# Kernel tuning notes

Measured on AMD Instinct MI355X. Metric: run time of the kernel, lower is better.

## Reference

```python
import jax, jax.numpy as jnp
import numpy as np

B, N, C, H, AD, HID = 2, 1024, 768, 12, 8, 3072
SCALE = (C // H) ** -0.5


def setup_inputs() -> dict:
    key = jax.random.key(0)
    ks = jax.random.split(key, 32)
    inp = {}
    for i in range(5):
        inp[f"x{i}"] = jax.random.normal(ks[i], (B, N, C), jnp.float32)
    def w(i, shape, s=0.02):
        return jax.random.normal(ks[i], shape, jnp.float32) * s
    inp.update({
        "ln1_g": jnp.ones((C,), jnp.float32), "ln1_b": jnp.zeros((C,), jnp.float32),
        "ln2_g": jnp.ones((C,), jnp.float32), "ln2_b": jnp.zeros((C,), jnp.float32),
        "qkv_w": w(5, (C, 3 * C)), "qkv_b": jnp.zeros((3 * C,), jnp.float32),
        "proj_w": w(6, (C, C)), "proj_b": jnp.zeros((C,), jnp.float32),
        "fc1_w": w(7, (C, HID)), "fc1_b": jnp.zeros((HID,), jnp.float32),
        "fc2_w": w(8, (HID, C)), "fc2_b": jnp.zeros((C,), jnp.float32),
        "at_dw": w(9, (C, AD)), "at_db": jnp.zeros((AD,), jnp.float32),
        "at_mw": w(10, (AD, AD)), "at_mb": jnp.zeros((AD,), jnp.float32),
        "at_uw": w(11, (AD, C)), "at_ub": jnp.zeros((C,), jnp.float32),
        "a2_dw": w(12, (C, AD)), "a2_db": jnp.zeros((AD,), jnp.float32),
        "a2_mw": w(13, (AD, AD)), "a2_mb": jnp.zeros((AD,), jnp.float32),
        "a2_uw": w(14, (AD, C)), "a2_ub": jnp.zeros((C,), jnp.float32),
    })
    return inp


def _ln(x, g, b, eps=1e-5):
    mu = x.mean(-1, keepdims=True)
    xc = x - mu
    var = (xc * xc).mean(-1, keepdims=True)
    return xc * jax.lax.rsqrt(var + eps) * g + b


def _adapter(x, dw, db, mw, mb, uw, ub):
    h = x @ dw + db          # bottleneck down [., AD]
    h = h @ mw + mb          # mid
    return h @ uw + ub       # up back to C


def _attn(x, qkv_w, qkv_b, proj_w, proj_b):
    # x: [S, B, N, C] (streams folded in leading axis)
    s, b, n, c = x.shape
    qkv = (x @ qkv_w + qkv_b).reshape(s, b, n, 3, H, c // H)
    q, k, v = jnp.moveaxis(qkv, 3, 0)            # each [S,B,N,H,D]
    scores = jnp.einsum('sbnhd,sbmhd->sbhnm', q * SCALE, k)  # fp32; clamp is a no-op
    p = jax.nn.softmax(scores, axis=-1)
    o = jnp.einsum('sbhnm,sbmhd->sbnhd', p, v).reshape(s, b, n, c)
    return o @ proj_w + proj_b


def reference(x0, x1, x2, x3, x4,
              ln1_g, ln1_b, ln2_g, ln2_b,
              qkv_w, qkv_b, proj_w, proj_b,
              fc1_w, fc1_b, fc2_w, fc2_b,
              at_dw, at_db, at_mw, at_mb, at_uw, at_ub,
              a2_dw, a2_db, a2_mw, a2_mb, a2_uw, a2_ub):
    xs = jnp.stack([x0, x1, x2, x3, x4])          # [5,B,N,C]
    n1 = _ln(xs, ln1_g, ln1_b)
    a1 = _adapter(n1, at_dw, at_db, at_mw, at_mb, at_uw, at_ub)
    ao = _attn(n1, qkv_w, qkv_b, proj_w, proj_b)
    # cross-stream residuals: x01=a1[0], x12=a1[1], ..., x10=a1[1], x21=a1[2], ...
    y0 = xs[0] + ao[0] + a1[1]
    y1 = xs[1] + ao[1] + a1[0] + a1[2]
    y2 = xs[2] + ao[2] + a1[1] + a1[3]
    y3 = xs[3] + ao[3] + a1[2] + a1[4]
    y4 = xs[4] + ao[4] + a1[3]
    ys = jnp.stack([y0, y1, y2, y3, y4])
    a2 = _adapter(_ln(ys, ln1_g, ln1_b), a2_dw, a2_db, a2_mw, a2_mb, a2_uw, a2_ub)
    h = _ln(ys, ln2_g, ln2_b) @ fc1_w + fc1_b
    m = jax.nn.gelu(h, approximate=False) @ fc2_w + fc2_b
    z0 = ys[0] + m[0] + a2[1]
    z1 = ys[1] + m[1] + a2[0] + a2[2]
    z2 = ys[2] + m[2] + a2[1] + a2[3]
    z3 = ys[3] + m[3] + a2[2] + a2[4]
    z4 = ys[4] + m[4] + a2[3]
    return jnp.stack([z0, z1, z2, z3, z4])        # [5,B,N,C]
```

## Files before the change

kernel.cpp:

```cpp
#include <hip/hip_runtime.h>
#include <math.h>

typedef __bf16 bf16;
typedef __attribute__((ext_vector_type(8))) __bf16 bf16x8;
typedef __attribute__((ext_vector_type(4))) __bf16 bf16x4;
typedef __attribute__((ext_vector_type(4))) float f32x4;
typedef __attribute__((ext_vector_type(16))) float f32x16;

#define TOK   10240
#define CD    768
#define NQKV  2304
#define NHID  3072
#define SEQ   1024
#define NH    12

__device__ __forceinline__ f32x4 mfma16(bf16x8 a, bf16x8 b, f32x4 c) {
  return __builtin_amdgcn_mfma_f32_16x16x32_bf16(a, b, c, 0, 0, 0);
}
__device__ __forceinline__ f32x16 mfma32(bf16x8 a, bf16x8 b, f32x16 c) {
  return __builtin_amdgcn_mfma_f32_32x32x16_bf16(a, b, c, 0, 0, 0);
}

__device__ __forceinline__ void gload16(const void* g, void* l) {
  __builtin_amdgcn_global_load_lds(
      (const __attribute__((address_space(1))) void*)g,
      (__attribute__((address_space(3))) void*)l, 16, 0, 0);
}

__device__ __forceinline__ unsigned pack2(bf16 a, bf16 b) {
  union { unsigned short u[2]; unsigned v; } x;
  x.u[0] = __builtin_bit_cast(unsigned short, a);
  x.u[1] = __builtin_bit_cast(unsigned short, b);
  return x.v;
}

__device__ __forceinline__ float fast_gelu(float v) {
  float u = 0.7978845608f * (v + 0.044715f * v * v * v);
  float e = __expf(fminf(2.f * u, 30.f));
  return 0.5f * v * (1.f + (e - 1.f) / (e + 1.f));
}

__global__ __launch_bounds__(256) void transpose_to_bf16(
    const float* __restrict__ in, bf16* __restrict__ out, int K, int N) {
  __shared__ float tile[32][33];
  const int bn = blockIdx.x * 32, bk = blockIdx.y * 32;
  const int r = threadIdx.x >> 5, c = threadIdx.x & 31;
#pragma unroll
  for (int i = 0; i < 4; ++i)
    tile[r + 8 * i][c] = in[(size_t)(bk + r + 8 * i) * N + bn + c];
  __syncthreads();
#pragma unroll
  for (int i = 0; i < 4; ++i)
    out[(size_t)(bn + r + 8 * i) * K + bk + c] = (bf16)tile[c][r + 8 * i];
}

__global__ __launch_bounds__(256) void ln5_kernel(
    const float* __restrict__ x0, const float* __restrict__ x1,
    const float* __restrict__ x2, const float* __restrict__ x3,
    const float* __restrict__ x4, const float* __restrict__ g,
    const float* __restrict__ b, bf16* __restrict__ out) {
  const int w = threadIdx.x >> 6, lane = threadIdx.x & 63;
  const int row = blockIdx.x * 4 + w;
  const int s = row >> 11, rem = row & 2047;
  const float* xp;
  switch (s) {
    case 0: xp = x0; break; case 1: xp = x1; break; case 2: xp = x2; break;
    case 3: xp = x3; break; default: xp = x4; break;
  }
  const f32x4* xr = (const f32x4*)(xp + (size_t)rem * CD);
  f32x4 v[3];
#pragma unroll
  for (int i = 0; i < 3; ++i) v[i] = xr[lane + 64 * i];
  float sum = 0.f;
#pragma unroll
  for (int i = 0; i < 3; ++i)
#pragma unroll
    for (int j = 0; j < 4; ++j) sum += v[i][j];
#pragma unroll
  for (int m = 32; m >= 1; m >>= 1) sum += __shfl_xor(sum, m);
  const float mu = sum * (1.f / 768.f);
  float vs = 0.f;
#pragma unroll
  for (int i = 0; i < 3; ++i)
#pragma unroll
    for (int j = 0; j < 4; ++j) { float d = v[i][j] - mu; vs += d * d; }
#pragma unroll
  for (int m = 32; m >= 1; m >>= 1) vs += __shfl_xor(vs, m);
  const float rstd = rsqrtf(vs * (1.f / 768.f) + 1e-5f);
  const f32x4* gp = (const f32x4*)g;
  const f32x4* bp = (const f32x4*)b;
  bf16* orow = out + (size_t)row * CD;
#pragma unroll
  for (int i = 0; i < 3; ++i) {
    const int c4 = lane + 64 * i;
    f32x4 gg = gp[c4], bb = bp[c4];
    bf16x4 o;
#pragma unroll
    for (int j = 0; j < 4; ++j)
      o[j] = (bf16)((v[i][j] - mu) * rstd * gg[j] + bb[j]);
    *(bf16x4*)(orow + c4 * 4) = o;
  }
}

__global__ __launch_bounds__(256) void fuse_res_ln(
    const float* __restrict__ x0, const float* __restrict__ x1,
    const float* __restrict__ x2, const float* __restrict__ x3,
    const float* __restrict__ x4, const float* __restrict__ add,
    const float* __restrict__ a, float* __restrict__ ys,
    const float* __restrict__ g1, const float* __restrict__ b1,
    const float* __restrict__ g2, const float* __restrict__ b2,
    bf16* __restrict__ o1, bf16* __restrict__ o2) {
  const int w = threadIdx.x >> 6, lane = threadIdx.x & 63;
  const int row = blockIdx.x * 4 + w;
  const int s = row >> 11, rem = row & 2047;
  const float* xp;
  switch (s) {
    case 0: xp = x0; break; case 1: xp = x1; break; case 2: xp = x2; break;
    case 3: xp = x3; break; default: xp = x4; break;
  }
  const f32x4* xr = (const f32x4*)(xp + (size_t)rem * CD);
  const f32x4* ar = (const f32x4*)(add + (size_t)row * CD);
  const f32x4* am = (const f32x4*)(a + (size_t)(row - 2048) * CD);
  const f32x4* ap = (const f32x4*)(a + (size_t)(row + 2048) * CD);
  f32x4 v[3];
#pragma unroll
  for (int i = 0; i < 3; ++i) {
    const int c4 = lane + 64 * i;
    f32x4 t = xr[c4] + ar[c4];
    if (s > 0) t += am[c4];
    if (s < 4) t += ap[c4];
    v[i] = t;
  }
  f32x4* yr = (f32x4*)(ys + (size_t)row * CD);
#pragma unroll
  for (int i = 0; i < 3; ++i) yr[lane + 64 * i] = v[i];

  float sum = 0.f;
#pragma unroll
  for (int i = 0; i < 3; ++i)
#pragma unroll
    for (int j = 0; j < 4; ++j) sum += v[i][j];
#pragma unroll
  for (int m = 32; m >= 1; m >>= 1) sum += __shfl_xor(sum, m);
  const float mu = sum * (1.f / 768.f);
  float vs = 0.f;
#pragma unroll
  for (int i = 0; i < 3; ++i)
#pragma unroll
    for (int j = 0; j < 4; ++j) { float d = v[i][j] - mu; vs += d * d; }
#pragma unroll
  for (int m = 32; m >= 1; m >>= 1) vs += __shfl_xor(vs, m);
  const float rstd = rsqrtf(vs * (1.f / 768.f) + 1e-5f);
  bf16* r1 = o1 + (size_t)row * CD;
  bf16* r2 = o2 + (size_t)row * CD;
#pragma unroll
  for (int i = 0; i < 3; ++i) {
    const int c4 = lane + 64 * i;
    f32x4 gg1 = ((const f32x4*)g1)[c4], bb1 = ((const f32x4*)b1)[c4];
    f32x4 gg2 = ((const f32x4*)g2)[c4], bb2 = ((const f32x4*)b2)[c4];
    bf16x4 oa, ob;
#pragma unroll
    for (int j = 0; j < 4; ++j) {
      float n = (v[i][j] - mu) * rstd;
      oa[j] = (bf16)(n * gg1[j] + bb1[j]);
      ob[j] = (bf16)(n * gg2[j] + bb2[j]);
    }
    *(bf16x4*)(r1 + c4 * 4) = oa;
    *(bf16x4*)(r2 + c4 * 4) = ob;
  }
}

template <int EPI>
__global__ __launch_bounds__(256) void gemm_bt(
    const bf16* __restrict__ A, const bf16* __restrict__ Bt,
    const float* __restrict__ bias, void* __restrict__ Cout, int N, int K,
    int nbn) {
  __shared__ bf16 As[2][4096];
  __shared__ bf16 Bs[2][4096];
  const int t = threadIdx.x, lane = t & 63, w = t >> 6;
  const int wm = w >> 1, wn = w & 1;

  const int chunk = gridDim.x >> 3;
  const int wg = (blockIdx.x & 7) * chunk + (blockIdx.x >> 3);
  const int bm = wg / nbn, bn = wg % nbn;

  f32x4 acc[4][4] = {};

  const int srow = t >> 2;
  const int scol = ((t & 3) ^ (srow & 3)) << 3;
  const bf16* a0 = A + (size_t)(bm * 128 + srow) * K + scol;
  const bf16* b0 = Bt + (size_t)(bn * 128 + srow) * K + scol;
  const size_t rstride = (size_t)64 * K;

  const int arow = wm * 64 + (lane & 15);
  const int brow = wn * 64 + (lane & 15);
  const int pch = (((lane >> 4) ^ (lane & 3)) << 3);

  gload16(a0, &As[0][w * 512]);
  gload16(a0 + rstride, &As[0][2048 + w * 512]);
  gload16(b0, &Bs[0][w * 512]);
  gload16(b0 + rstride, &Bs[0][2048 + w * 512]);
  __syncthreads();

  int cur = 0;
  for (int kt = 0; kt < K; kt += 32) {
    if (kt + 32 < K) {
      const bf16* ak = a0 + kt + 32;
      const bf16* bk = b0 + kt + 32;
      gload16(ak, &As[cur ^ 1][w * 512]);
      gload16(ak + rstride, &As[cur ^ 1][2048 + w * 512]);
      gload16(bk, &Bs[cur ^ 1][w * 512]);
      gload16(bk + rstride, &Bs[cur ^ 1][2048 + w * 512]);
    }
    bf16x8 af[4], bfr[4];
#pragma unroll
    for (int f = 0; f < 4; ++f) {
      af[f] = *(const bf16x8*)&As[cur][(arow + f * 16) * 32 + pch];
      bfr[f] = *(const bf16x8*)&Bs[cur][(brow + f * 16) * 32 + pch];
    }
#pragma unroll
    for (int mf = 0; mf < 4; ++mf)
#pragma unroll
      for (int nf = 0; nf < 4; ++nf)
        acc[mf][nf] = mfma16(af[mf], bfr[nf], acc[mf][nf]);
    __syncthreads();
    cur ^= 1;
  }

#pragma unroll
  for (int mf = 0; mf < 4; ++mf) {
    const int grow0 = bm * 128 + wm * 64 + mf * 16 + (lane >> 4) * 4;
#pragma unroll
    for (int nf = 0; nf < 4; ++nf) {
      const int gcol = bn * 128 + wn * 64 + nf * 16 + (lane & 15);
      const float bv = bias[gcol];
#pragma unroll
      for (int r = 0; r < 4; ++r) {
        float v = acc[mf][nf][r] + bv;
        if (EPI == 2) v = fast_gelu(v);
        const size_t idx = (size_t)(grow0 + r) * N + gcol;
        if (EPI == 0) ((float*)Cout)[idx] = v;
        else ((bf16*)Cout)[idx] = (bf16)v;
      }
    }
  }
}

__global__ __launch_bounds__(256, 3) void attn_v2(
    const bf16* __restrict__ qkv, bf16* __restrict__ obuf) {
  __shared__ bf16 Ks[2][4096];
  __shared__ bf16 Vt[2][4096];
  const int t = threadIdx.x, lane = t & 63, w = t >> 6;
  const int g = lane >> 5, q32 = lane & 31, rq7 = q32 & 7;

  const int xcd = blockIdx.x & 7, slot = blockIdx.x >> 3;
  const int work = xcd * 120 + slot;
  const int sbh = work >> 3, qt = work & 7;
  const int sb = sbh / NH, h = sbh % NH;
  const size_t tokbase = (size_t)sb * SEQ;
  const int qoff = h * 64, koff = CD + h * 64, voff = 2 * CD + h * 64;

  const int qrow = qt * 128 + w * 32 + q32;
  bf16x8 qf[4];
  {
    const bf16* qp = qkv + (tokbase + qrow) * NQKV + qoff + g * 8;
#pragma unroll
    for (int kd = 0; kd < 4; ++kd) {
      bf16x8 v = *(const bf16x8*)(qp + kd * 16);
#pragma unroll
      for (int j = 0; j < 8; ++j) v[j] = (bf16)((float)v[j] * 0.125f);
      qf[kd] = v;
    }
  }

  const int skv1 = t >> 3, sc1 = (t & 7) ^ (skv1 & 7);
  const int skv2 = (t + 256) >> 3, sc2 = (t & 7) ^ (skv2 & 7);
  const int vkv0 = 2 * (t & 31);
  const int vd0 = 8 * (t >> 5);
  const int c0 = (vkv0 & 51) | ((vkv0 & 4) << 1) | ((vkv0 & 8) >> 1);
  const int vchunk = c0 >> 3, vsub = c0 & 7;
  const bf16* kbase = qkv + tokbase * NQKV + koff;
  const bf16* vbase = qkv + tokbase * NQKV + voff;

  {
    const bf16* kb0 = kbase;
    gload16(kb0 + (size_t)skv1 * NQKV + sc1 * 8, &Ks[0][w * 512]);
    gload16(kb0 + (size_t)skv2 * NQKV + sc2 * 8, &Ks[0][2048 + w * 512]);
    const bf16* vp = vbase + (size_t)vkv0 * NQKV + vd0;
    bf16x8 r0 = *(const bf16x8*)vp;
    bf16x8 r1 = *(const bf16x8*)(vp + NQKV);
#pragma unroll
    for (int j = 0; j < 8; ++j) {
      const int d = vd0 + j;
      *(unsigned*)&Vt[0][d * 64 + ((vchunk ^ j) << 3) + vsub] =
          pack2(r0[j], r1[j]);
    }
  }
  __syncthreads();

  float m_run = -1e30f, l_run = 0.f;
  f32x16 oT0 = {}, oT1 = {};
  int cur = 0;

  for (int kt = 0; kt < 16; ++kt) {
    bf16x8 nv0, nv1;
    if (kt < 15) {
      const bf16* vp = vbase + (size_t)((kt + 1) * 64 + vkv0) * NQKV + vd0;
      nv0 = *(const bf16x8*)vp;
      nv1 = *(const bf16x8*)(vp + NQKV);
      const bf16* kb0 = kbase + (size_t)(kt + 1) * 64 * NQKV;
      gload16(kb0 + (size_t)skv1 * NQKV + sc1 * 8, &Ks[cur ^ 1][w * 512]);
      gload16(kb0 + (size_t)skv2 * NQKV + sc2 * 8,
              &Ks[cur ^ 1][2048 + w * 512]);
    }

    f32x16 sT0 = {}, sT1 = {};
#pragma unroll
    for (int kd = 0; kd < 4; ++kd) {
      bf16x8 kf0 =
          *(const bf16x8*)&Ks[cur][q32 * 64 + (((2 * kd + g) ^ rq7) << 3)];
      bf16x8 kf1 = *(const bf16x8*)&Ks[cur][(32 + q32) * 64 +
                                            (((2 * kd + g) ^ rq7) << 3)];
      sT0 = mfma32(kf0, qf[kd], sT0);
      sT1 = mfma32(kf1, qf[kd], sT1);
    }

    float mt = sT0[0];
#pragma unroll
    for (int r = 1; r < 16; ++r) mt = fmaxf(mt, sT0[r]);
#pragma unroll
    for (int r = 0; r < 16; ++r) mt = fmaxf(mt, sT1[r]);
    mt = fmaxf(mt, __shfl_xor(mt, 32));
    const float mnew = fmaxf(m_run, mt);
    const float alpha = __expf(m_run - mnew);
    m_run = mnew;
    float rs = 0.f;
#pragma unroll
    for (int r = 0; r < 16; ++r) {
      sT0[r] = __expf(sT0[r] - mnew);
      rs += sT0[r];
    }
#pragma unroll
    for (int r = 0; r < 16; ++r) {
      sT1[r] = __expf(sT1[r] - mnew);
      rs += sT1[r];
    }
    rs += __shfl_xor(rs, 32);
    l_run = l_run * alpha + rs;
#pragma unroll
    for (int r = 0; r < 16; ++r) { oT0[r] *= alpha; oT1[r] *= alpha; }

    bf16x8 pa[4];
#pragma unroll
    for (int hh = 0; hh < 2; ++hh)
#pragma unroll
      for (int j = 0; j < 8; ++j) {
        pa[hh][j] = (bf16)sT0[8 * hh + j];
        pa[2 + hh][j] = (bf16)sT1[8 * hh + j];
      }

#pragma unroll
    for (int ks = 0; ks < 4; ++ks) {
      bf16x8 vf0 =
          *(const bf16x8*)&Vt[cur][q32 * 64 + (((2 * ks + g) ^ rq7) << 3)];
      bf16x8 vf1 = *(const bf16x8*)&Vt[cur][(32 + q32) * 64 +
                                            (((2 * ks + g) ^ rq7) << 3)];
      oT0 = mfma32(vf0, pa[ks], oT0);
      oT1 = mfma32(vf1, pa[ks], oT1);
    }

    if (kt < 15) {
#pragma unroll
      for (int j = 0; j < 8; ++j) {
        const int d = vd0 + j;
        *(unsigned*)&Vt[cur ^ 1][d * 64 + ((vchunk ^ j) << 3) + vsub] =
            pack2(nv0[j], nv1[j]);
      }
    }
    __syncthreads();
    cur ^= 1;
  }

  const float rl = 1.f / l_run;
  bf16* orow = obuf + (tokbase + qrow) * CD + h * 64;
#pragma unroll
  for (int m = 0; m < 4; ++m) {
    bf16x4 o0, o1;
#pragma unroll
    for (int r = 0; r < 4; ++r) {
      o0[r] = (bf16)(oT0[4 * m + r] * rl);
      o1[r] = (bf16)(oT1[4 * m + r] * rl);
    }
    *(bf16x4*)(orow + 8 * m + 4 * g) = o0;
    *(bf16x4*)(orow + 32 + 8 * m + 4 * g) = o1;
  }
}

__global__ __launch_bounds__(256) void adapter_kernel(
    const bf16* __restrict__ X, const float* __restrict__ dw,
    const float* __restrict__ db, const float* __restrict__ mw,
    const float* __restrict__ mb, const float* __restrict__ uw,
    const float* __restrict__ ub, float* __restrict__ out) {
  const int tok = blockIdx.x * 4 + (threadIdx.x >> 6);
  const int lane = threadIdx.x & 63;
  const bf16* xr = X + (size_t)tok * CD;
  float xv[12];
#pragma unroll
  for (int i = 0; i < 12; ++i) xv[i] = (float)xr[lane + 64 * i];
  float h1[8] = {0, 0, 0, 0, 0, 0, 0, 0};
#pragma unroll
  for (int i = 0; i < 12; ++i) {
    const f32x4* dr = (const f32x4*)(dw + (size_t)(lane + 64 * i) * 8);
    f32x4 d0 = dr[0], d1 = dr[1];
#pragma unroll
    for (int j = 0; j < 4; ++j) {
      h1[j] += xv[i] * d0[j];
      h1[4 + j] += xv[i] * d1[j];
    }
  }
#pragma unroll
  for (int m = 1; m < 64; m <<= 1)
#pragma unroll
    for (int j = 0; j < 8; ++j) h1[j] += __shfl_xor(h1[j], m);
#pragma unroll
  for (int j = 0; j < 8; ++j) h1[j] += db[j];
  float h2[8];
#pragma unroll
  for (int k = 0; k < 8; ++k) {
    float v = mb[k];
#pragma unroll
    for (int j = 0; j < 8; ++j) v += h1[j] * mw[j * 8 + k];
    h2[k] = v;
  }
#pragma unroll
  for (int i = 0; i < 12; ++i) {
    const int c = lane + 64 * i;
    float v = ub[c];
#pragma unroll
    for (int k = 0; k < 8; ++k) v += h2[k] * uw[k * CD + c];
    out[(size_t)tok * CD + c] = v;
  }
}

__global__ __launch_bounds__(256) void cross_residual(
    const float* __restrict__ p0, const float* __restrict__ p1,
    const float* __restrict__ p2, const float* __restrict__ p3,
    const float* __restrict__ p4, const float* __restrict__ add,
    const float* __restrict__ a, float* __restrict__ out) {
  const int s = blockIdx.y;
  const size_t i = (size_t)blockIdx.x * 256 + threadIdx.x;
  const size_t spitch = (size_t)2048 * 768 / 4;
  const size_t sb = (size_t)s * spitch;
  const float* p;
  switch (s) {
    case 0: p = p0; break; case 1: p = p1; break; case 2: p = p2; break;
    case 3: p = p3; break; default: p = p4; break;
  }
  f32x4 v = ((const f32x4*)p)[i];
  v += ((const f32x4*)add)[sb + i];
  if (s > 0) v += ((const f32x4*)a)[sb - spitch + i];
  if (s < 4) v += ((const f32x4*)a)[sb + spitch + i];
  ((f32x4*)out)[sb + i] = v;
}

#define OFF_WTQKV  ((size_t)0)
#define OFF_WTPROJ ((size_t)3538944)
#define OFF_WTFC1  ((size_t)4718592)
#define OFF_WTFC2  ((size_t)9437184)
#define OFF_N1     ((size_t)14155776)
#define OFF_BIG    ((size_t)29884416)
#define OFF_OBUF   ((size_t)77070336)
#define OFF_AOM    ((size_t)92798976)
#define OFF_A12    ((size_t)124256256)
#define OFF_YS     ((size_t)155713536)
#define OFF_L2Y    ((size_t)187170816)

extern "C" void kernel_launch(void* const* d_in, const int* in_sizes, int n_in,
                              void* d_out, int out_size, void* d_ws,
                              size_t ws_size, hipStream_t stream) {
  const float* x0 = (const float*)d_in[0];
  const float* x1 = (const float*)d_in[1];
  const float* x2 = (const float*)d_in[2];
  const float* x3 = (const float*)d_in[3];
  const float* x4 = (const float*)d_in[4];
  const float* ln1_g = (const float*)d_in[5];
  const float* ln1_b = (const float*)d_in[6];
  const float* ln2_g = (const float*)d_in[7];
  const float* ln2_b = (const float*)d_in[8];
  const float* qkv_w = (const float*)d_in[9];
  const float* qkv_b = (const float*)d_in[10];
  const float* proj_w = (const float*)d_in[11];
  const float* proj_b = (const float*)d_in[12];
  const float* fc1_w = (const float*)d_in[13];
  const float* fc1_b = (const float*)d_in[14];
  const float* fc2_w = (const float*)d_in[15];
  const float* fc2_b = (const float*)d_in[16];
  const float* at_dw = (const float*)d_in[17];
  const float* at_db = (const float*)d_in[18];
  const float* at_mw = (const float*)d_in[19];
  const float* at_mb = (const float*)d_in[20];
  const float* at_uw = (const float*)d_in[21];
  const float* at_ub = (const float*)d_in[22];
  const float* a2_dw = (const float*)d_in[23];
  const float* a2_db = (const float*)d_in[24];
  const float* a2_mw = (const float*)d_in[25];
  const float* a2_mb = (const float*)d_in[26];
  const float* a2_uw = (const float*)d_in[27];
  const float* a2_ub = (const float*)d_in[28];

  char* ws = (char*)d_ws;
  bf16* wt_qkv = (bf16*)(ws + OFF_WTQKV);
  bf16* wt_proj = (bf16*)(ws + OFF_WTPROJ);
  bf16* wt_fc1 = (bf16*)(ws + OFF_WTFC1);
  bf16* wt_fc2 = (bf16*)(ws + OFF_WTFC2);
  bf16* n1 = (bf16*)(ws + OFF_N1);
  bf16* qkvb = (bf16*)(ws + OFF_BIG);
  bf16* obuf = (bf16*)(ws + OFF_OBUF);
  float* aom = (float*)(ws + OFF_AOM);
  float* a12 = (float*)(ws + OFF_A12);
  float* ysb = (float*)(ws + OFF_YS);
  bf16* l2y = (bf16*)(ws + OFF_L2Y);

  const dim3 b256(256);

  transpose_to_bf16<<<dim3(72, 24), b256, 0, stream>>>(qkv_w, wt_qkv, 768, 2304);
  transpose_to_bf16<<<dim3(24, 24), b256, 0, stream>>>(proj_w, wt_proj, 768, 768);
  transpose_to_bf16<<<dim3(96, 24), b256, 0, stream>>>(fc1_w, wt_fc1, 768, 3072);
  transpose_to_bf16<<<dim3(24, 96), b256, 0, stream>>>(fc2_w, wt_fc2, 3072, 768);

  ln5_kernel<<<2560, b256, 0, stream>>>(x0, x1, x2, x3, x4, ln1_g, ln1_b, n1);

  gemm_bt<1><<<1440, b256, 0, stream>>>(n1, wt_qkv, qkv_b, qkvb, NQKV, 768, 18);

  adapter_kernel<<<2560, b256, 0, stream>>>(n1, at_dw, at_db, at_mw, at_mb,
                                            at_uw, at_ub, a12);

  attn_v2<<<960, b256, 0, stream>>>(qkvb, obuf);

  gemm_bt<0><<<480, b256, 0, stream>>>(obuf, wt_proj, proj_b, aom, CD, 768, 6);

  fuse_res_ln<<<2560, b256, 0, stream>>>(x0, x1, x2, x3, x4, aom, a12, ysb,
                                         ln1_g, ln1_b, ln2_g, ln2_b, n1, l2y);

  adapter_kernel<<<2560, b256, 0, stream>>>(n1, a2_dw, a2_db, a2_mw, a2_mb,
                                            a2_uw, a2_ub, a12);

  gemm_bt<2><<<1920, b256, 0, stream>>>(l2y, wt_fc1, fc1_b, qkvb, NHID, 768, 24);

  gemm_bt<0><<<480, b256, 0, stream>>>(qkvb, wt_fc2, fc2_b, aom, CD, NHID, 6);

  const size_t sp = (size_t)2048 * 768;
  cross_residual<<<dim3(1536, 5), b256, 0, stream>>>(
      ysb, ysb + sp, ysb + 2 * sp, ysb + 3 * sp, ysb + 4 * sp, aom, a12,
      (float*)d_out);
}
```

Baseline: 405.2 us.

## Replace 128x128 GEMM with 256x256-tile 8-wave ping-pong pipelined GEMM

Replaces the 128x128, K=32 double-buffered GEMM with a 256x256 tile, K=64 kernel using 512 threads. The main loop is split into barrier-separated phases that interleave LDS fragment loads, async global-to-LDS staging and MFMA bursts under raised wave priority. The larger tiles are meant to cut global and LDS traffic per FLOP and hide load latency behind compute. In exchange the grids become small (120 blocks for the 768-wide GEMMs), which risks leaving CUs idle on a 256-CU part, and the kernel uses 128KB of LDS per block.

```diff
diff --git a/kernel.cpp b/kernel.cpp
--- a/kernel.cpp
+++ b/kernel.cpp
@@ -170,73 +170,147 @@
   }
 }
 
+#define GBAR() __builtin_amdgcn_s_barrier()
+
+#define LOADA(MH, BUF)                                                      \
+  _Pragma("unroll") for (int m_ = 0; m_ < 4; ++m_) {                        \
+    af[m_][0] =                                                             \
+        *(const bf16x8*)&As[BUF][((MH)*128 + arow + m_ * 16) * 64 + ach0];  \
+    af[m_][1] =                                                             \
+        *(const bf16x8*)&As[BUF][((MH)*128 + arow + m_ * 16) * 64 + ach1];  \
+  }
+
+#define LOADB(DST, NH, BUF)                                                 \
+  _Pragma("unroll") for (int n_ = 0; n_ < 2; ++n_) {                        \
+    DST[n_][0] =                                                            \
+        *(const bf16x8*)&Bs[BUF][(brow + (NH)*32 + n_ * 16) * 64 + ach0];   \
+    DST[n_][1] =                                                            \
+        *(const bf16x8*)&Bs[BUF][(brow + (NH)*32 + n_ * 16) * 64 + ach1];   \
+  }
+
+#define MFMA_PH(MH, NH, BF)                                                 \
+  __builtin_amdgcn_s_setprio(1);                                            \
+  _Pragma("unroll") for (int m_ = 0; m_ < 4; ++m_)                          \
+  _Pragma("unroll") for (int n_ = 0; n_ < 2; ++n_) {                        \
+    acc[(MH)*4 + m_][(NH)*2 + n_] =                                         \
+        mfma16(af[m_][0], BF[n_][0], acc[(MH)*4 + m_][(NH)*2 + n_]);        \
+    acc[(MH)*4 + m_][(NH)*2 + n_] =                                         \
+        mfma16(af[m_][1], BF[n_][1], acc[(MH)*4 + m_][(NH)*2 + n_]);        \
+  }                                                                         \
+  __builtin_amdgcn_s_setprio(0);
+
 template <int EPI>
-__global__ __launch_bounds__(256) void gemm_bt(
+__global__ __launch_bounds__(512, 2) void gemm256(
     const bf16* __restrict__ A, const bf16* __restrict__ Bt,
     const float* __restrict__ bias, void* __restrict__ Cout, int N, int K,
     int nbn) {
-  __shared__ bf16 As[2][4096];
-  __shared__ bf16 Bs[2][4096];
+  __shared__ bf16 As[2][16384];
+  __shared__ bf16 Bs[2][16384];
   const int t = threadIdx.x, lane = t & 63, w = t >> 6;
-  const int wm = w >> 1, wn = w & 1;
-
-  const int chunk = gridDim.x >> 3;
-  const int wg = (blockIdx.x & 7) * chunk + (blockIdx.x >> 3);
+  const int wm = w >> 2, wn = w & 3;
+
+  const int chunkg = gridDim.x >> 3;
+  const int wg = (blockIdx.x & 7) * chunkg + (blockIdx.x >> 3);
   const int bm = wg / nbn, bn = wg % nbn;
 
-  f32x4 acc[4][4] = {};
-
-  const int srow = t >> 2;
-  const int scol = ((t & 3) ^ (srow & 3)) << 3;
-  const bf16* a0 = A + (size_t)(bm * 128 + srow) * K + scol;
-  const bf16* b0 = Bt + (size_t)(bn * 128 + srow) * K + scol;
-  const size_t rstride = (size_t)64 * K;
+  f32x4 acc[8][4] = {};
+
+  const int srow = t >> 3;
+  const int scol = ((t & 7) ^ (srow & 7)) << 3;
+  const bf16* Ab = A + (size_t)(bm * 256 + srow) * K + scol;
+  const bf16* Bb = Bt + (size_t)(bn * 256 + srow) * K + scol;
+  const size_t r64 = (size_t)64 * K;
+
+  auto stage_a = [&](int buf, int h, int kt) {
+    const bf16* g = Ab + (size_t)h * 128 * K + (size_t)kt * 64;
+    gload16(g, &As[buf][h * 8192 + w * 512]);
+    gload16(g + r64, &As[buf][h * 8192 + 4096 + w * 512]);
+  };
+  auto stage_b = [&](int buf, int h, int kt) {
+    const bf16* g = Bb + (size_t)h * 128 * K + (size_t)kt * 64;
+    gload16(g, &Bs[buf][h * 8192 + w * 512]);
+    gload16(g + r64, &Bs[buf][h * 8192 + 4096 + w * 512]);
+  };
 
   const int arow = wm * 64 + (lane & 15);
   const int brow = wn * 64 + (lane & 15);
-  const int pch = (((lane >> 4) ^ (lane & 3)) << 3);
-
-  gload16(a0, &As[0][w * 512]);
-  gload16(a0 + rstride, &As[0][2048 + w * 512]);
-  gload16(b0, &Bs[0][w * 512]);
-  gload16(b0 + rstride, &Bs[0][2048 + w * 512]);
-  __syncthreads();
-
-  int cur = 0;
-  for (int kt = 0; kt < K; kt += 32) {
-    if (kt + 32 < K) {
-      const bf16* ak = a0 + kt + 32;
-      const bf16* bk = b0 + kt + 32;
-      gload16(ak, &As[cur ^ 1][w * 512]);
-      gload16(ak + rstride, &As[cur ^ 1][2048 + w * 512]);
-      gload16(bk, &Bs[cur ^ 1][w * 512]);
-      gload16(bk + rstride, &Bs[cur ^ 1][2048 + w * 512]);
-    }
-    bf16x8 af[4], bfr[4];
-#pragma unroll
-    for (int f = 0; f < 4; ++f) {
-      af[f] = *(const bf16x8*)&As[cur][(arow + f * 16) * 32 + pch];
-      bfr[f] = *(const bf16x8*)&Bs[cur][(brow + f * 16) * 32 + pch];
-    }
-#pragma unroll
-    for (int mf = 0; mf < 4; ++mf)
-#pragma unroll
-      for (int nf = 0; nf < 4; ++nf)
-        acc[mf][nf] = mfma16(af[mf], bfr[nf], acc[mf][nf]);
-    __syncthreads();
-    cur ^= 1;
-  }
-
-#pragma unroll
-  for (int mf = 0; mf < 4; ++mf) {
-    const int grow0 = bm * 128 + wm * 64 + mf * 16 + (lane >> 4) * 4;
-#pragma unroll
-    for (int nf = 0; nf < 4; ++nf) {
-      const int gcol = bn * 128 + wn * 64 + nf * 16 + (lane & 15);
+  const int ach0 = (((lane >> 4) + 0) ^ (lane & 7)) << 3;
+  const int ach1 = (((lane >> 4) + 4) ^ (lane & 7)) << 3;
+
+  stage_a(0, 0, 0); stage_b(0, 0, 0); stage_b(0, 1, 0); stage_a(0, 1, 0);
+  stage_a(1, 0, 1); stage_b(1, 0, 1);
+  asm volatile("s_waitcnt vmcnt(4)" ::: "memory");
+  GBAR();
+
+  const int NT = K >> 6, NI = NT >> 1;
+  bf16x8 af[4][2], bf0[2][2], bf1[2][2];
+
+  for (int j = 0; j < NI; ++j) {
+    const int tA = 2 * j, tB = 2 * j + 1;
+    const bool notlast = (j + 1 < NI);
+
+    LOADA(0, 0);
+    LOADB(bf0, 0, 0);
+    stage_b(1, 1, tB);
+    GBAR();
+    MFMA_PH(0, 0, bf0);
+    GBAR();
+    LOADB(bf1, 1, 0);
+    stage_a(1, 1, tB);
+    GBAR();
+    MFMA_PH(0, 1, bf1);
+    GBAR();
+    LOADA(1, 0);
+    if (notlast) stage_a(0, 0, tA + 2);
+    GBAR();
+    MFMA_PH(1, 0, bf0);
+    GBAR();
+    if (notlast) {
+      stage_b(0, 0, tA + 2);
+      asm volatile("s_waitcnt vmcnt(4)" ::: "memory");
+    } else {
+      asm volatile("s_waitcnt vmcnt(0)" ::: "memory");
+    }
+    GBAR();
+    MFMA_PH(1, 1, bf1);
+    GBAR();
+
+    LOADA(0, 1);
+    LOADB(bf0, 0, 1);
+    if (notlast) stage_b(0, 1, tA + 2);
+    GBAR();
+    MFMA_PH(0, 0, bf0);
+    GBAR();
+    LOADB(bf1, 1, 1);
+    if (notlast) stage_a(0, 1, tA + 2);
+    GBAR();
+    MFMA_PH(0, 1, bf1);
+    GBAR();
+    LOADA(1, 1);
+    if (notlast) stage_a(1, 0, tB + 2);
+    GBAR();
+    MFMA_PH(1, 0, bf0);
+    GBAR();
+    if (notlast) {
+      stage_b(1, 0, tB + 2);
+      asm volatile("s_waitcnt vmcnt(4)" ::: "memory");
+    }
+    GBAR();
+    MFMA_PH(1, 1, bf1);
+    GBAR();
+  }
+
+#pragma unroll
+  for (int am = 0; am < 8; ++am) {
+    const int grow0 =
+        bm * 256 + (am >> 2) * 128 + wm * 64 + (am & 3) * 16 + (lane >> 4) * 4;
+#pragma unroll
+    for (int an = 0; an < 4; ++an) {
+      const int gcol = bn * 256 + wn * 64 + an * 16 + (lane & 15);
       const float bv = bias[gcol];
 #pragma unroll
       for (int r = 0; r < 4; ++r) {
-        float v = acc[mf][nf][r] + bv;
+        float v = acc[am][an][r] + bv;
         if (EPI == 2) v = fast_gelu(v);
         const size_t idx = (size_t)(grow0 + r) * N + gcol;
         if (EPI == 0) ((float*)Cout)[idx] = v;
@@ -522,6 +596,7 @@
   bf16* l2y = (bf16*)(ws + OFF_L2Y);
 
   const dim3 b256(256);
+  const dim3 b512(512);
 
   transpose_to_bf16<<<dim3(72, 24), b256, 0, stream>>>(qkv_w, wt_qkv, 768, 2304);
   transpose_to_bf16<<<dim3(24, 24), b256, 0, stream>>>(proj_w, wt_proj, 768, 768);
@@ -530,14 +605,14 @@
 
   ln5_kernel<<<2560, b256, 0, stream>>>(x0, x1, x2, x3, x4, ln1_g, ln1_b, n1);
 
-  gemm_bt<1><<<1440, b256, 0, stream>>>(n1, wt_qkv, qkv_b, qkvb, NQKV, 768, 18);
+  gemm256<1><<<360, b512, 0, stream>>>(n1, wt_qkv, qkv_b, qkvb, NQKV, 768, 9);
 
   adapter_kernel<<<2560, b256, 0, stream>>>(n1, at_dw, at_db, at_mw, at_mb,
                                             at_uw, at_ub, a12);
 
   attn_v2<<<960, b256, 0, stream>>>(qkvb, obuf);
 
-  gemm_bt<0><<<480, b256, 0, stream>>>(obuf, wt_proj, proj_b, aom, CD, 768, 6);
+  gemm256<0><<<120, b512, 0, stream>>>(obuf, wt_proj, proj_b, aom, CD, 768, 3);
 
   fuse_res_ln<<<2560, b256, 0, stream>>>(x0, x1, x2, x3, x4, aom, a12, ysb,
                                          ln1_g, ln1_b, ln2_g, ln2_b, n1, l2y);
@@ -545,9 +620,9 @@
   adapter_kernel<<<2560, b256, 0, stream>>>(n1, a2_dw, a2_db, a2_mw, a2_mb,
                                             a2_uw, a2_ub, a12);
 
-  gemm_bt<2><<<1920, b256, 0, stream>>>(l2y, wt_fc1, fc1_b, qkvb, NHID, 768, 24);
-
-  gemm_bt<0><<<480, b256, 0, stream>>>(qkvb, wt_fc2, fc2_b, aom, CD, NHID, 6);
+  gemm256<2><<<480, b512, 0, stream>>>(l2y, wt_fc1, fc1_b, qkvb, NHID, 768, 12);
+
+  gemm256<0><<<120, b512, 0, stream>>>(qkvb, wt_fc2, fc2_b, aom, CD, NHID, 3);
 
   const size_t sp = (size_t)2048 * 768;
   cross_residual<<<dim3(1536, 5), b256, 0, stream>>>(
```

Result: slower. 416.2 us (+2.7%).
